# Kernel optimization log

Hardware: AMD Instinct MI355X
Metric: run time of the kernel (lower is better)

Reference implementation:

```python
import jax, jax.numpy as jnp
import numpy as np

B, S, D, H = 2, 2048, 1024, 16
HD = D // H  # 64
NEG = 1.0e9


def setup_inputs() -> dict:
    key = jax.random.key(0)
    ks = jax.random.split(key, 9)
    scale = 1.0 / np.sqrt(D)
    return {
        "q_in": jax.random.normal(ks[0], (B, S, D), jnp.float32),
        "k_in": jax.random.normal(ks[1], (B, S, D), jnp.float32),
        "v_in": jax.random.normal(ks[2], (B, S, D), jnp.float32),
        "Wq": jax.random.normal(ks[3], (D, D), jnp.float32) * scale,
        "bq": jnp.zeros((D,), jnp.float32),
        "Wk": jax.random.normal(ks[4], (D, D), jnp.float32) * scale,
        "bk": jnp.zeros((D,), jnp.float32),
        "Wv": jax.random.normal(ks[5], (D, D), jnp.float32) * scale,
        "bv": jnp.zeros((D,), jnp.float32),
        "Wo": jax.random.normal(ks[6], (D, D), jnp.float32) * scale,
        "bo": jnp.zeros((D,), jnp.float32),
    }


def _split_heads(x):
    # [B,S,D] -> [B,H,S,HD]
    return x.reshape(B, S, H, HD).transpose(0, 2, 1, 3)


def reference(q_in, k_in, v_in, Wq, bq, Wk, bk, Wv, bv, Wo, bo):
    q = _split_heads(q_in @ Wq + bq)
    k = _split_heads(k_in @ Wk + bk)
    v = _split_heads(v_in @ Wv + bv)
    # scaled dot-product attention with additive causal mask (use_causal_mask=True)
    scores = jnp.einsum("bhqd,bhkd->bhqk", q, k) / jnp.sqrt(jnp.float32(HD))
    causal = jnp.tril(jnp.ones((S, S), jnp.float32))  # band_part(ones, -1, 0)
    scores = scores + (causal - 1.0) * NEG
    weights = jax.nn.softmax(scores, axis=-1)
    attn = jnp.einsum("bhqk,bhkd->bhqd", weights, v)
    concat = attn.transpose(0, 2, 1, 3).reshape(B, S, D)
    return concat @ Wo + bo
```

## Files before the change

### kernel.cpp

```cpp
#include <hip/hip_runtime.h>

#define B_  2
#define S_  2048
#define D_  1024
#define H_  16
#define HD_ 64
#define MM  (B_ * S_)

typedef __bf16 bf16;
typedef __attribute__((ext_vector_type(8))) __bf16 bf16x8;
typedef __attribute__((ext_vector_type(4))) __bf16 bf16x4;
typedef __attribute__((ext_vector_type(4))) float  f32x4;

__device__ inline float exp2g(float x) { return __builtin_amdgcn_exp2f(x); }

__device__ inline bf16x8 load8(const bf16* p) { return *(const bf16x8*)p; }
__device__ inline bf16x8 load8(const float* p) {
  float4 a = *(const float4*)p;
  float4 b = *(const float4*)(p + 4);
  bf16x8 r;
  r[0] = (bf16)a.x; r[1] = (bf16)a.y; r[2] = (bf16)a.z; r[3] = (bf16)a.w;
  r[4] = (bf16)b.x; r[5] = (bf16)b.y; r[6] = (bf16)b.z; r[7] = (bf16)b.w;
  return r;
}

__device__ inline void gld16(void* lds, const void* g) {
  __builtin_amdgcn_global_load_lds(
      (const __attribute__((address_space(1))) unsigned int*)g,
      (__attribute__((address_space(3))) unsigned int*)lds, 16, 0, 0);
}

__global__ __launch_bounds__(256) void transpose_w(
    const float* __restrict__ W0, const float* __restrict__ W1,
    const float* __restrict__ W2, const float* __restrict__ W3,
    bf16* __restrict__ T0, bf16* __restrict__ T1,
    bf16* __restrict__ T2, bf16* __restrict__ T3,
    const float* __restrict__ X0, const float* __restrict__ X1,
    const float* __restrict__ X2,
    bf16* __restrict__ Y0, bf16* __restrict__ Y1, bf16* __restrict__ Y2) {
  const int z = blockIdx.z;
  if (z >= 4) {
    const int p = z - 4, t = p >> 2;
    const float* src = t == 0 ? X0 : t == 1 ? X1 : X2;
    bf16* dst = t == 0 ? Y0 : t == 1 ? Y1 : Y2;
    long base = ((long)(p & 3) << 20) +
                (long)(blockIdx.y * 32 + blockIdx.x) * 1024 + threadIdx.x * 4;
    float4 v = *(const float4*)&src[base];
    bf16x4 o4;
    o4[0] = (bf16)v.x; o4[1] = (bf16)v.y; o4[2] = (bf16)v.z; o4[3] = (bf16)v.w;
    *(bf16x4*)&dst[base] = o4;
    return;
  }
  __shared__ bf16 t[32][40];
  const float* in = z == 0 ? W0 : z == 1 ? W1 : z == 2 ? W2 : W3;
  bf16* out = z == 0 ? T0 : z == 1 ? T1 : z == 2 ? T2 : T3;
  const int tx = threadIdx.x & 31;
  const int ty = threadIdx.x >> 5;
  const int r0 = blockIdx.y * 32, c0 = blockIdx.x * 32;
#pragma unroll
  for (int j = 0; j < 32; j += 8)
    t[ty + j][tx] = (bf16)in[(long)(r0 + ty + j) * D_ + (c0 + tx)];
  __syncthreads();
#pragma unroll
  for (int j = 0; j < 32; j += 8)
    out[(long)(c0 + ty + j) * D_ + (r0 + tx)] = t[tx][ty + j];
}

__global__ __launch_bounds__(256) void transpose_v64(const bf16* __restrict__ V,
                                                     bf16* __restrict__ VT) {
  __shared__ bf16 t[64][72];
  const int tid = threadIdx.x;
  const int s0 = blockIdx.x * 64;
  const int bh = blockIdx.y;
  const int b = bh >> 4, h = bh & 15;
  const bf16* ip = V + (long)b * S_ * D_ + h * HD_;
  bf16* op = VT + (long)bh * HD_ * S_;
#pragma unroll
  for (int i = 0; i < 2; ++i) {
    int c = tid + i * 256;
    int r = c >> 3, cc = (c & 7) * 8;
    *(bf16x8*)&t[r][cc] = *(const bf16x8*)&ip[(long)(s0 + r) * D_ + cc];
  }
  __syncthreads();
#pragma unroll
  for (int i = 0; i < 2; ++i) {
    int c = tid + i * 256;
    int d = c >> 3, sc = (c & 7) * 8;
    bf16x8 v;
#pragma unroll
    for (int j = 0; j < 8; ++j) v[j] = t[sc + j][d];
    *(bf16x8*)&op[(long)d * S_ + s0 + sc] = v;
  }
}

template <typename AT, typename OT>
__global__ __launch_bounds__(256) void gemm_bt_dma(
    const AT* __restrict__ A0, const AT* __restrict__ A1, const AT* __restrict__ A2,
    const bf16* __restrict__ B0, const bf16* __restrict__ B1, const bf16* __restrict__ B2,
    const float* __restrict__ c0, const float* __restrict__ c1, const float* __restrict__ c2,
    OT* __restrict__ C0, OT* __restrict__ C1, OT* __restrict__ C2,
    int M, int N, int K) {
  __shared__ bf16 lA[128][32];
  __shared__ bf16 lB[128][32];
  const int z = blockIdx.z;
  const AT*    A    = z == 0 ? A0 : z == 1 ? A1 : A2;
  const bf16*  Bt   = z == 0 ? B0 : z == 1 ? B1 : B2;
  const float* bias = z == 0 ? c0 : z == 1 ? c1 : c2;
  OT*          C    = z == 0 ? C0 : z == 1 ? C1 : C2;

  const int tid = threadIdx.x;
  const int lane = tid & 63, wave = tid >> 6;
  const int quad = lane >> 4, l16 = lane & 15;
  const int bm = blockIdx.y * 128, bn = blockIdx.x * 128;
  const int wm = (wave >> 1) * 64, wn = (wave & 1) * 64;

  f32x4 acc[4][4] = {};

  for (int k0 = 0; k0 < K; k0 += 32) {
    __syncthreads();
#pragma unroll
    for (int i = 0; i < 2; ++i) {
      const int nbase = wave * 128 + i * 64;
      const int n = nbase + lane;
      const int row = n >> 2, kc = (n & 3) * 8;
      gld16(&lB[0][0] + (long)nbase * 8, &Bt[(long)(bn + row) * K + k0 + kc]);
      if constexpr (__is_same(AT, bf16))
        gld16(&lA[0][0] + (long)nbase * 8, &A[(long)(bm + row) * K + k0 + kc]);
    }
    if constexpr (!__is_same(AT, bf16)) {
#pragma unroll
      for (int i = 0; i < 2; ++i) {
        int c = tid + i * 256;
        int row = c >> 2, kc = (c & 3) * 8;
        *(bf16x8*)&lA[row][kc] = load8(&A[(long)(bm + row) * K + k0 + kc]);
      }
    }
    __syncthreads();
    bf16x8 af[4], bfr[4];
#pragma unroll
    for (int i = 0; i < 4; ++i) {
      af[i]  = *(const bf16x8*)&lA[wm + i * 16 + l16][quad * 8];
      bfr[i] = *(const bf16x8*)&lB[wn + i * 16 + l16][quad * 8];
    }
#pragma unroll
    for (int mi = 0; mi < 4; ++mi)
#pragma unroll
      for (int ni = 0; ni < 4; ++ni)
        acc[mi][ni] = __builtin_amdgcn_mfma_f32_16x16x32_bf16(af[mi], bfr[ni],
                                                              acc[mi][ni], 0, 0, 0);
  }

#pragma unroll
  for (int mi = 0; mi < 4; ++mi)
#pragma unroll
    for (int ni = 0; ni < 4; ++ni) {
      int col = bn + wn + ni * 16 + l16;
      float bv = bias[col];
#pragma unroll
      for (int r = 0; r < 4; ++r) {
        int row = bm + wm + mi * 16 + quad * 4 + r;
        C[(long)row * N + col] = (OT)(acc[mi][ni][r] + bv);
      }
    }
}

__global__ __launch_bounds__(256) void gemm_bt_64(const bf16* __restrict__ A,
                                                  const bf16* __restrict__ Bt,
                                                  const float* __restrict__ bias,
                                                  float* __restrict__ C,
                                                  int M, int N, int K) {
  __shared__ bf16 lA[128][32];
  __shared__ bf16 lB[64][32];
  const int tid = threadIdx.x;
  const int lane = tid & 63, wave = tid >> 6;
  const int quad = lane >> 4, l16 = lane & 15;
  const int bm = blockIdx.y * 128, bn = blockIdx.x * 64;
  const int wm = (wave >> 1) * 64, wn = (wave & 1) * 32;

  f32x4 acc[4][2] = {};

  for (int k0 = 0; k0 < K; k0 += 32) {
    __syncthreads();
#pragma unroll
    for (int i = 0; i < 2; ++i) {
      const int nbase = wave * 128 + i * 64;
      const int n = nbase + lane;
      const int row = n >> 2, kc = (n & 3) * 8;
      gld16(&lA[0][0] + (long)nbase * 8, &A[(long)(bm + row) * K + k0 + kc]);
    }
    {
      const int nbase = wave * 64;
      const int n = nbase + lane;
      const int row = n >> 2, kc = (n & 3) * 8;
      gld16(&lB[0][0] + (long)nbase * 8, &Bt[(long)(bn + row) * K + k0 + kc]);
    }
    __syncthreads();
    bf16x8 af[4], bfr[2];
#pragma unroll
    for (int i = 0; i < 4; ++i)
      af[i] = *(const bf16x8*)&lA[wm + i * 16 + l16][quad * 8];
#pragma unroll
    for (int i = 0; i < 2; ++i)
      bfr[i] = *(const bf16x8*)&lB[wn + i * 16 + l16][quad * 8];
#pragma unroll
    for (int mi = 0; mi < 4; ++mi)
#pragma unroll
      for (int ni = 0; ni < 2; ++ni)
        acc[mi][ni] = __builtin_amdgcn_mfma_f32_16x16x32_bf16(af[mi], bfr[ni],
                                                              acc[mi][ni], 0, 0, 0);
  }

#pragma unroll
  for (int mi = 0; mi < 4; ++mi)
#pragma unroll
    for (int ni = 0; ni < 2; ++ni) {
      int col = bn + wn + ni * 16 + l16;
      float bv = bias[col];
#pragma unroll
      for (int r = 0; r < 4; ++r) {
        int row = bm + wm + mi * 16 + quad * 4 + r;
        C[(long)row * N + col] = acc[mi][ni][r] + bv;
      }
    }
}

#define SCALE_LOG2E 0.1803368801111244f

__device__ inline void attn_step5(bool diag, int qloc, int quad, int l16,
                                  const bf16 (*lKb)[64], const bf16 (*lVb)[64],
                                  bf16 (*lpw)[72], const bf16x8* aq,
                                  f32x4* o, float& l_s) {
  const int sw = l16 & 7;
  f32x4 s[4];
#pragma unroll
  for (int ni = 0; ni < 4; ++ni) {
    f32x4 a = {};
#pragma unroll
    for (int c = 0; c < 2; ++c) {
      bf16x8 kf = *(const bf16x8*)&lKb[ni * 16 + l16][((c * 4 + quad) ^ sw) * 8];
      a = __builtin_amdgcn_mfma_f32_16x16x32_bf16(kf, aq[c], a, 0, 0, 0);
    }
    s[ni] = a * SCALE_LOG2E;
  }
  if (diag) {
#pragma unroll
    for (int ni = 0; ni < 4; ++ni)
#pragma unroll
      for (int r = 0; r < 4; ++r)
        if (ni * 16 + quad * 4 + r > qloc) s[ni][r] = -1e9f;
  }
  float rs = 0.f;
#pragma unroll
  for (int ni = 0; ni < 4; ++ni) {
    bf16x4 p4;
#pragma unroll
    for (int r = 0; r < 4; ++r) {
      float p = exp2g(s[ni][r]);
      p4[r] = (bf16)p;
      rs += p;
    }
    *(bf16x4*)&lpw[l16][ni * 16 + quad * 4] = p4;
  }
  l_s += rs;
#pragma unroll
  for (int c = 0; c < 2; ++c) {
    bf16x8 ap = *(const bf16x8*)&lpw[l16][c * 32 + quad * 8];
#pragma unroll
    for (int di = 0; di < 4; ++di) {
      bf16x8 vf = *(const bf16x8*)&lVb[di * 16 + l16][((c * 4 + quad) ^ sw) * 8];
      o[di] = __builtin_amdgcn_mfma_f32_16x16x32_bf16(vf, ap, o[di], 0, 0, 0);
    }
  }
}

__device__ inline void store_o(bf16* Ob, int qrow, int lane, int quad, int l16,
                               bf16 (*lpw)[72], const f32x4* o, float l_s) {
  float rs = l_s;
  rs += __shfl_xor(rs, 16);
  rs += __shfl_xor(rs, 32);
  const float inv = 1.0f / rs;
#pragma unroll
  for (int di = 0; di < 4; ++di) {
    bf16x4 p4;
#pragma unroll
    for (int r = 0; r < 4; ++r) p4[r] = (bf16)(o[di][r] * inv);
    *(bf16x4*)&lpw[l16][di * 16 + quad * 4] = p4;
  }
  const int q = lane >> 2, db = (lane & 3) * 16;
  bf16x8 v0 = *(const bf16x8*)&lpw[q][db];
  bf16x8 v1 = *(const bf16x8*)&lpw[q][db + 8];
  *(bf16x8*)&Ob[(long)(qrow + q) * D_ + db] = v0;
  *(bf16x8*)&Ob[(long)(qrow + q) * D_ + db + 8] = v1;
}

__global__ __launch_bounds__(512) void flash_attn5(const bf16* __restrict__ Q,
                                                   const bf16* __restrict__ K,
                                                   const bf16* __restrict__ VT,
                                                   bf16* __restrict__ O) {
  __shared__ bf16 lK[2][64][64];
  __shared__ bf16 lV[2][64][64];
  __shared__ bf16 lp[8][16][72];
  const int tid = threadIdx.x;
  const int lane = tid & 63, wave = tid >> 6;
  const int quad = lane >> 4, l16 = lane & 15;
  const int x = blockIdx.x, bh = blockIdx.y;
  const int qtA = x, qtB = 31 - x;
  const bool isB = wave >= 4;
  const int w4 = wave & 3;
  const int myqt = isB ? qtB : qtA;
  const int b = bh >> 4, h = bh & 15;
  const bf16* Qb = Q + (long)b * S_ * D_ + h * HD_;
  const bf16* Kb = K + (long)b * S_ * D_ + h * HD_;
  const bf16* Vb = VT + (long)bh * HD_ * S_;
  const int qrow = myqt * 64 + w4 * 16;
  const int qloc = w4 * 16 + l16;

  bf16x8 aq[2];
#pragma unroll
  for (int c = 0; c < 2; ++c)
    aq[c] = *(const bf16x8*)&Qb[(long)(qrow + l16) * D_ + c * 32 + quad * 8];

  f32x4 o[4] = {};
  float l_s = 0.f;

  const int srow = tid >> 3, scol = tid & 7;
  const int swcol = (scol ^ (srow & 7)) * 8;

  bf16x8 kreg, vreg;
  kreg = *(const bf16x8*)&Kb[(long)srow * D_ + scol * 8];
  vreg = *(const bf16x8*)&Vb[(long)srow * S_ + scol * 8];
  *(bf16x8*)&lK[0][srow][swcol] = kreg;
  *(bf16x8*)&lV[0][srow][swcol] = vreg;
  __syncthreads();

  const int ktMax = qtB;
  for (int kt = 0; kt <= ktMax; ++kt) {
    const int p = kt & 1;
    if (kt < ktMax) {
      const long k0 = (long)(kt + 1) * 64;
      kreg = *(const bf16x8*)&Kb[(k0 + srow) * D_ + scol * 8];
      vreg = *(const bf16x8*)&Vb[(long)srow * S_ + k0 + scol * 8];
    }
    if (isB || kt <= qtA)
      attn_step5(kt == myqt, qloc, quad, l16, lK[p], lV[p], lp[wave], aq,
                 o, l_s);
    if (kt < ktMax) {
      *(bf16x8*)&lK[1 - p][srow][swcol] = kreg;
      *(bf16x8*)&lV[1 - p][srow][swcol] = vreg;
      __syncthreads();
    }
  }

  bf16* Ob = O + (long)b * S_ * D_ + h * HD_;
  store_o(Ob, qrow, lane, quad, l16, lp[wave], o, l_s);
}

extern "C" void kernel_launch(void* const* d_in, const int* in_sizes, int n_in,
                              void* d_out, int out_size, void* d_ws, size_t ws_size,
                              hipStream_t stream) {
  (void)in_sizes; (void)n_in; (void)out_size;
  const float* q_in = (const float*)d_in[0];
  const float* k_in = (const float*)d_in[1];
  const float* v_in = (const float*)d_in[2];
  const float* Wq   = (const float*)d_in[3];
  const float* bq   = (const float*)d_in[4];
  const float* Wk   = (const float*)d_in[5];
  const float* bk   = (const float*)d_in[6];
  const float* Wv   = (const float*)d_in[7];
  const float* bv   = (const float*)d_in[8];
  const float* Wo   = (const float*)d_in[9];
  const float* bo   = (const float*)d_in[10];
  float* out = (float*)d_out;

  bf16* ws = (bf16*)d_ws;
  const size_t WSZ = (size_t)D_ * D_;
  const size_t TSZ = (size_t)B_ * S_ * D_;
  bf16* WqT = ws;
  bf16* WkT = WqT + WSZ;
  bf16* WvT = WkT + WSZ;
  bf16* WoT = WvT + WSZ;
  bf16* Qp  = WoT + WSZ;
  bf16* Kp  = Qp + TSZ;
  bf16* Vp  = Kp + TSZ;
  bf16* VTp = Vp + TSZ;
  bf16* Ap  = VTp + TSZ;
  bf16* Xq  = VTp;
  bf16* Xk  = Ap;
  bf16* Xv  = Ap + TSZ;
  const bool pre = ws_size >= (4 * WSZ + 6 * TSZ) * sizeof(bf16);

  dim3 blk(256);
  transpose_w<<<dim3(32, 32, pre ? 16 : 4), blk, 0, stream>>>(
      Wq, Wk, Wv, Wo, WqT, WkT, WvT, WoT, q_in, k_in, v_in, Xq, Xk, Xv);

  if (pre)
    gemm_bt_dma<bf16, bf16><<<dim3(8, 32, 3), blk, 0, stream>>>(
        Xq, Xk, Xv, WqT, WkT, WvT, bq, bk, bv, Qp, Kp, Vp, MM, D_, D_);
  else
    gemm_bt_dma<float, bf16><<<dim3(8, 32, 3), blk, 0, stream>>>(
        q_in, k_in, v_in, WqT, WkT, WvT, bq, bk, bv, Qp, Kp, Vp, MM, D_, D_);

  transpose_v64<<<dim3(S_ / 64, B_ * H_), blk, 0, stream>>>(Vp, VTp);

  flash_attn5<<<dim3(16, B_ * H_), dim3(512), 0, stream>>>(Qp, Kp, VTp, Ap);

  gemm_bt_64<<<dim3(16, 32), blk, 0, stream>>>(Ap, WoT, bo, out, MM, D_, D_);
}
```

Measured before the change: 229.1 us.

## Split each key tile across wave halves so all eight waves stay busy

Before, four waves served the low query tile and four the high one, so the low-tile waves sat idle once their causal range ended. Now both query tiles are walked in one 33-step sequence over all needed key tiles. Each half of the block computes scores and PV for 32 of the 64 keys in a tile. At the end the two halves' partial outputs and row sums are combined through shared memory. The goal is to remove idle waves and give every block the same loop length, at the cost of extra register state for two accumulators and a final reduction step.

```diff
diff --git a/kernel.cpp b/kernel.cpp
--- a/kernel.cpp
+++ b/kernel.cpp
@@ -226,50 +226,49 @@
 
 #define SCALE_LOG2E 0.1803368801111244f
 
-__device__ inline void attn_step5(bool diag, int qloc, int quad, int l16,
+__device__ inline void attn_step7(bool diag, int qloc, int kh, int quad,
+                                  int l16,
                                   const bf16 (*lKb)[64], const bf16 (*lVb)[64],
                                   bf16 (*lpw)[72], const bf16x8* aq,
                                   f32x4* o, float& l_s) {
   const int sw = l16 & 7;
-  f32x4 s[4];
-#pragma unroll
-  for (int ni = 0; ni < 4; ++ni) {
+  f32x4 s[2];
+#pragma unroll
+  for (int i = 0; i < 2; ++i) {
+    const int ni = 2 * kh + i;
     f32x4 a = {};
 #pragma unroll
     for (int c = 0; c < 2; ++c) {
       bf16x8 kf = *(const bf16x8*)&lKb[ni * 16 + l16][((c * 4 + quad) ^ sw) * 8];
       a = __builtin_amdgcn_mfma_f32_16x16x32_bf16(kf, aq[c], a, 0, 0, 0);
     }
-    s[ni] = a * SCALE_LOG2E;
+    s[i] = a * SCALE_LOG2E;
   }
   if (diag) {
 #pragma unroll
-    for (int ni = 0; ni < 4; ++ni)
+    for (int i = 0; i < 2; ++i)
 #pragma unroll
       for (int r = 0; r < 4; ++r)
-        if (ni * 16 + quad * 4 + r > qloc) s[ni][r] = -1e9f;
+        if ((2 * kh + i) * 16 + quad * 4 + r > qloc) s[i][r] = -1e9f;
   }
   float rs = 0.f;
 #pragma unroll
-  for (int ni = 0; ni < 4; ++ni) {
+  for (int i = 0; i < 2; ++i) {
     bf16x4 p4;
 #pragma unroll
     for (int r = 0; r < 4; ++r) {
-      float p = exp2g(s[ni][r]);
+      float p = exp2g(s[i][r]);
       p4[r] = (bf16)p;
       rs += p;
     }
-    *(bf16x4*)&lpw[l16][ni * 16 + quad * 4] = p4;
+    *(bf16x4*)&lpw[l16][(2 * kh + i) * 16 + quad * 4] = p4;
   }
   l_s += rs;
-#pragma unroll
-  for (int c = 0; c < 2; ++c) {
-    bf16x8 ap = *(const bf16x8*)&lpw[l16][c * 32 + quad * 8];
-#pragma unroll
-    for (int di = 0; di < 4; ++di) {
-      bf16x8 vf = *(const bf16x8*)&lVb[di * 16 + l16][((c * 4 + quad) ^ sw) * 8];
-      o[di] = __builtin_amdgcn_mfma_f32_16x16x32_bf16(vf, ap, o[di], 0, 0, 0);
-    }
+  bf16x8 ap = *(const bf16x8*)&lpw[l16][kh * 32 + quad * 8];
+#pragma unroll
+  for (int di = 0; di < 4; ++di) {
+    bf16x8 vf = *(const bf16x8*)&lVb[di * 16 + l16][((kh * 4 + quad) ^ sw) * 8];
+    o[di] = __builtin_amdgcn_mfma_f32_16x16x32_bf16(vf, ap, o[di], 0, 0, 0);
   }
 }
 
@@ -293,35 +292,36 @@
   *(bf16x8*)&Ob[(long)(qrow + q) * D_ + db + 8] = v1;
 }
 
-__global__ __launch_bounds__(512) void flash_attn5(const bf16* __restrict__ Q,
+__global__ __launch_bounds__(512) void flash_attn7(const bf16* __restrict__ Q,
                                                    const bf16* __restrict__ K,
                                                    const bf16* __restrict__ VT,
                                                    bf16* __restrict__ O) {
-  __shared__ bf16 lK[2][64][64];
-  __shared__ bf16 lV[2][64][64];
+  __shared__ bf16 lKV[2][2][64][64];
   __shared__ bf16 lp[8][16][72];
+  __shared__ float lsum[512];
   const int tid = threadIdx.x;
   const int lane = tid & 63, wave = tid >> 6;
   const int quad = lane >> 4, l16 = lane & 15;
+  const int qgroup = wave & 3, kh = wave >> 2;
   const int x = blockIdx.x, bh = blockIdx.y;
   const int qtA = x, qtB = 31 - x;
-  const bool isB = wave >= 4;
-  const int w4 = wave & 3;
-  const int myqt = isB ? qtB : qtA;
   const int b = bh >> 4, h = bh & 15;
   const bf16* Qb = Q + (long)b * S_ * D_ + h * HD_;
   const bf16* Kb = K + (long)b * S_ * D_ + h * HD_;
   const bf16* Vb = VT + (long)bh * HD_ * S_;
-  const int qrow = myqt * 64 + w4 * 16;
-  const int qloc = w4 * 16 + l16;
-
-  bf16x8 aq[2];
-#pragma unroll
-  for (int c = 0; c < 2; ++c)
-    aq[c] = *(const bf16x8*)&Qb[(long)(qrow + l16) * D_ + c * 32 + quad * 8];
-
-  f32x4 o[4] = {};
-  float l_s = 0.f;
+  const int qrowA = qtA * 64 + qgroup * 16;
+  const int qrowB = qtB * 64 + qgroup * 16;
+  const int qloc = qgroup * 16 + l16;
+
+  bf16x8 aqA[2], aqB[2];
+#pragma unroll
+  for (int c = 0; c < 2; ++c) {
+    aqA[c] = *(const bf16x8*)&Qb[(long)(qrowA + l16) * D_ + c * 32 + quad * 8];
+    aqB[c] = *(const bf16x8*)&Qb[(long)(qrowB + l16) * D_ + c * 32 + quad * 8];
+  }
+
+  f32x4 oA[4] = {}, oB[4] = {};
+  float lA = 0.f, lB = 0.f;
 
   const int srow = tid >> 3, scol = tid & 7;
   const int swcol = (scol ^ (srow & 7)) * 8;
@@ -329,30 +329,68 @@
   bf16x8 kreg, vreg;
   kreg = *(const bf16x8*)&Kb[(long)srow * D_ + scol * 8];
   vreg = *(const bf16x8*)&Vb[(long)srow * S_ + scol * 8];
-  *(bf16x8*)&lK[0][srow][swcol] = kreg;
-  *(bf16x8*)&lV[0][srow][swcol] = vreg;
+  *(bf16x8*)&lKV[0][0][srow][swcol] = kreg;
+  *(bf16x8*)&lKV[1][0][srow][swcol] = vreg;
   __syncthreads();
 
-  const int ktMax = qtB;
-  for (int kt = 0; kt <= ktMax; ++kt) {
-    const int p = kt & 1;
-    if (kt < ktMax) {
-      const long k0 = (long)(kt + 1) * 64;
+  for (int t = 0; t <= 32; ++t) {
+    const int p = t & 1;
+    if (t < 32) {
+      const int g = (t + 1 <= qtA) ? (t + 1) : (t - qtA);
+      const long k0 = (long)g * 64;
       kreg = *(const bf16x8*)&Kb[(k0 + srow) * D_ + scol * 8];
       vreg = *(const bf16x8*)&Vb[(long)srow * S_ + k0 + scol * 8];
     }
-    if (isB || kt <= qtA)
-      attn_step5(kt == myqt, qloc, quad, l16, lK[p], lV[p], lp[wave], aq,
-                 o, l_s);
-    if (kt < ktMax) {
-      *(bf16x8*)&lK[1 - p][srow][swcol] = kreg;
-      *(bf16x8*)&lV[1 - p][srow][swcol] = vreg;
+    if (t <= qtA)
+      attn_step7(t == qtA, qloc, kh, quad, l16, lKV[0][p], lKV[1][p],
+                 lp[qgroup], aqA, oA, lA);
+    else
+      attn_step7(t == 32, qloc, kh, quad, l16, lKV[0][p], lKV[1][p],
+                 lp[qgroup], aqB, oB, lB);
+    if (t < 32) {
+      *(bf16x8*)&lKV[0][1 - p][srow][swcol] = kreg;
+      *(bf16x8*)&lKV[1][1 - p][srow][swcol] = vreg;
       __syncthreads();
     }
   }
 
+  __syncthreads();
+  float* scrO = (float*)lKV;
+  const int pairid = qgroup * 64 + lane;
+  if (kh == 1) {
+#pragma unroll
+    for (int di = 0; di < 4; ++di)
+#pragma unroll
+      for (int r = 0; r < 4; ++r)
+        scrO[pairid * 16 + di * 4 + r] = oA[di][r];
+    lsum[pairid] = lA;
+  } else {
+#pragma unroll
+    for (int di = 0; di < 4; ++di)
+#pragma unroll
+      for (int r = 0; r < 4; ++r)
+        scrO[4096 + pairid * 16 + di * 4 + r] = oB[di][r];
+    lsum[256 + pairid] = lB;
+  }
+  __syncthreads();
   bf16* Ob = O + (long)b * S_ * D_ + h * HD_;
-  store_o(Ob, qrow, lane, quad, l16, lp[wave], o, l_s);
+  if (kh == 0) {
+#pragma unroll
+    for (int di = 0; di < 4; ++di)
+#pragma unroll
+      for (int r = 0; r < 4; ++r)
+        oA[di][r] += scrO[pairid * 16 + di * 4 + r];
+    lA += lsum[pairid];
+    store_o(Ob, qrowA, lane, quad, l16, lp[wave], oA, lA);
+  } else {
+#pragma unroll
+    for (int di = 0; di < 4; ++di)
+#pragma unroll
+      for (int r = 0; r < 4; ++r)
+        oB[di][r] += scrO[4096 + pairid * 16 + di * 4 + r];
+    lB += lsum[256 + pairid];
+    store_o(Ob, qrowB, lane, quad, l16, lp[wave], oB, lB);
+  }
 }
 
 extern "C" void kernel_launch(void* const* d_in, const int* in_sizes, int n_in,
@@ -402,7 +440,7 @@
 
   transpose_v64<<<dim3(S_ / 64, B_ * H_), blk, 0, stream>>>(Vp, VTp);
 
-  flash_attn5<<<dim3(16, B_ * H_), dim3(512), 0, stream>>>(Qp, Kp, VTp, Ap);
+  flash_attn7<<<dim3(16, B_ * H_), dim3(512), 0, stream>>>(Qp, Kp, VTp, Ap);
 
   gemm_bt_64<<<dim3(16, 32), blk, 0, stream>>>(Ap, WoT, bo, out, MM, D_, D_);
 }
```

New measurement: 231.3 us. About the same (+1.0%).
